# Kernel optimization log

Measured on AMD Instinct MI355X. Metric: run time of the kernel, lower is better.

The kernel has to match this reference:

```python
import jax, jax.numpy as jnp
import numpy as np

TEMP = 0.5  # init kwarg `tmp`
NUM_CLASSES = 100


def setup_inputs() -> dict:
    key = jax.random.key(0)
    k1, k2 = jax.random.split(key)
    embedding = jax.random.normal(k1, (8192, 256), dtype=jnp.float32)
    label = jax.random.randint(k2, (8192,), 0, NUM_CLASSES, dtype=jnp.int64)
    return {"embedding": embedding, "label": label}


def reference(embedding, label):
    # Row-normalize -> pairwise cosine similarity [N, N]
    normed = embedding / jnp.linalg.norm(embedding, axis=1, keepdims=True)
    sim = (normed @ normed.T) / TEMP  # already divided by temperature

    N = embedding.shape[0]
    eye = jnp.eye(N, dtype=bool)

    # Denominator: sum of exp(sim) over off-diagonal entries per row
    exp_sim = jnp.exp(sim)
    row_sum = jnp.sum(jnp.where(eye, 0.0, exp_sim), axis=1)  # [N]

    # log(exp(sim_ij) / row_sum_i) = sim_ij - log(row_sum_i)
    log_prob = sim - jnp.log(row_sum)[:, None]

    # Positive mask: same label, i != j
    pos_mask = (label[:, None] == label[None, :]) & ~eye
    n_i = jnp.sum(pos_mask, axis=1)  # positives per anchor

    inner = jnp.sum(jnp.where(pos_mask, log_prob, 0.0), axis=1)  # [N]
    per_anchor = jnp.where(n_i > 0, -inner / jnp.maximum(n_i, 1).astype(sim.dtype), 0.0)
    return jnp.sum(per_anchor)
```

## Files before the change

### kernel.cpp

```cpp
#include <hip/hip_runtime.h>
#include <hip/hip_bf16.h>
#include <stdint.h>

#define N    8192
#define D    256
#define NCLS 100

static constexpr float TEMP    = 0.5f;
static constexpr float SCALE_F = 1.69864360f;
static constexpr float LN2     = 0.69314718055994531f;

typedef float f32x4 __attribute__((ext_vector_type(4)));

__device__ __forceinline__ unsigned short f2bf(float f) {
  union { float f; unsigned int u; } x; x.f = f;
  unsigned int r = x.u + 0x7fffu + ((x.u >> 16) & 1u);
  return (unsigned short)(r >> 16);
}
__device__ __forceinline__ float bf2f(unsigned short b) {
  union { unsigned int u; float f; } x; x.u = ((unsigned int)b) << 16;
  return x.f;
}
__device__ __forceinline__ void gld16(const void* g, void* l) {
  __builtin_amdgcn_global_load_lds(
      (const __attribute__((address_space(1))) unsigned int*)g,
      (__attribute__((address_space(3))) unsigned int*)l, 16, 0, 0);
}


__global__ __launch_bounds__(256) void normalize_kernel(
    const float* __restrict__ emb, const long long* __restrict__ label,
    unsigned short* __restrict__ abf, unsigned char* __restrict__ a8,
    float* __restrict__ rowsum, int* __restrict__ cnt,
    int* __restrict__ list) {
  const int row  = blockIdx.x * 4 + (threadIdx.x >> 6);
  const int lane = threadIdx.x & 63;
  const float4 v = ((const float4*)(emb + (size_t)row * D))[lane];
  float ss = v.x * v.x + v.y * v.y + v.z * v.z + v.w * v.w;
#pragma unroll
  for (int off = 1; off < 64; off <<= 1) ss += __shfl_xor(ss, off);
  const float s = rsqrtf(ss) * SCALE_F;
  const float x = v.x * s, y = v.y * s, z = v.z * s, wv = v.w * s;

  ushort4 o;
  o.x = f2bf(x); o.y = f2bf(y); o.z = f2bf(z); o.w = f2bf(wv);
  ((ushort4*)(abf + (size_t)row * D))[lane] = o;

  int p = __builtin_amdgcn_cvt_pk_fp8_f32(x, y, 0, false);
  p = __builtin_amdgcn_cvt_pk_fp8_f32(z, wv, p, true);
  *(int*)(a8 + (size_t)(row >> 4) * 4096 + (lane >> 1) * 128 +
          (row & 15) * 8 + (lane & 1) * 4) = p;

  if (lane == 0) {
    rowsum[row] = 0.f;
    const int c = (int)label[row];
    const int slot = atomicAdd(cnt + c, 1);
    list[c * 256 + slot] = row;
  }
}

#define TM 128
#define TN 128
#define JT 4

__global__ __launch_bounds__(256, 3) void simexp_rowsum_kernel(
    const unsigned char* __restrict__ A, float* __restrict__ rowsum) {
  __shared__ __align__(16) unsigned char sa[TM * 256];
  const int tid  = threadIdx.x;
  const int w    = tid >> 6;
  const int lane = tid & 63;
  const int quad = lane >> 4;
  const int l15  = lane & 15;

  const int b = blockIdx.x;
  int x = (int)((-1.0f + sqrtf(1.0f + 2.0f * (float)b)) * 0.5f);
  while (2 * (x + 1) * (x + 1) + 2 * (x + 1) <= b) ++x;
  while (2 * x * x + 2 * x > b) --x;
  const int y = b - (2 * x * x + 2 * x);

  const int row0 = y * TM;
  const int jc0  = x * (TN * JT);
  const int sdiag = (y >= 4 * x) ? (y - 4 * x) : -1;
  const int jt0   = (sdiag >= 0) ? sdiag : 0;
  const int pr0 = row0 >> 4;
  const int pam = (w & 1) * 4;
  const int pbn = (w >> 1) * 4;
  const int wm  = (w & 1) * 64;
  const int jn0 = (w >> 1) * 64;

#pragma unroll
  for (int p = 0; p < 8; ++p) {
    const int seg = w * 8 + p;
    gld16(A + (size_t)(pr0 + (seg >> 2)) * 4096 + (seg & 3) * 1024 + lane * 16,
          sa + seg * 1024);
  }
  __syncthreads();

  float rowpart[4][4];
#pragma unroll
  for (int mt = 0; mt < 4; ++mt)
#pragma unroll
    for (int e = 0; e < 4; ++e) rowpart[mt][e] = 0.f;

  for (int jt = jt0; jt < JT; ++jt) {
    const unsigned char* Bp =
        A + (size_t)(((jc0 + jt * TN) >> 4) + pbn) * 4096;

    f32x4 acc[4][4];
#pragma unroll
    for (int mt = 0; mt < 4; ++mt)
#pragma unroll
      for (int nt = 0; nt < 4; ++nt) acc[mt][nt] = (f32x4){0.f, 0.f, 0.f, 0.f};

#pragma unroll
    for (int kq = 0; kq < 4; ++kq) {
#pragma unroll
      for (int kkl = 0; kkl < 2; ++kkl) {
        const int fo = (kkl * 4 + quad) * 128 + l15 * 8;
        long af[4], bf[4];
#pragma unroll
        for (int nt = 0; nt < 4; ++nt)
          bf[nt] = *(const long*)(Bp + nt * 4096 + kq * 1024 + fo);
#pragma unroll
        for (int mt = 0; mt < 4; ++mt)
          af[mt] = *(const long*)(sa + (pam + mt) * 4096 + kq * 1024 + fo);
#pragma unroll
        for (int mt = 0; mt < 4; ++mt)
#pragma unroll
          for (int nt = 0; nt < 4; ++nt)
            acc[mt][nt] = __builtin_amdgcn_mfma_f32_16x16x32_fp8_fp8(
                af[mt], bf[nt], acc[mt][nt], 0, 0, 0);
      }
    }

    const bool diag = (jt == sdiag);
    float colpart[4] = {0.f, 0.f, 0.f, 0.f};
#pragma unroll
    for (int mt = 0; mt < 4; ++mt)
#pragma unroll
      for (int nt = 0; nt < 4; ++nt)
#pragma unroll
        for (int e = 0; e < 4; ++e) {
          float v = __builtin_amdgcn_exp2f(acc[mt][nt][e]);
          if (diag) {
            const int iloc = wm + mt * 16 + quad * 4 + e;
            const int jloc = jn0 + nt * 16 + l15;
            v = (iloc < jloc) ? v : 0.f;
          }
          rowpart[mt][e] += v;
          colpart[nt] += v;
        }
#pragma unroll
    for (int nt = 0; nt < 4; ++nt) {
      float v = colpart[nt];
      v += __shfl_xor(v, 16);
      v += __shfl_xor(v, 32);
      if (quad == 0)
        atomicAdd(&rowsum[jc0 + jt * TN + jn0 + nt * 16 + l15], v);
    }
  }

#pragma unroll
  for (int mt = 0; mt < 4; ++mt)
#pragma unroll
    for (int e = 0; e < 4; ++e) {
      float v = rowpart[mt][e];
      v += __shfl_xor(v, 1);
      v += __shfl_xor(v, 2);
      v += __shfl_xor(v, 4);
      v += __shfl_xor(v, 8);
      if (l15 == 0)
        atomicAdd(&rowsum[row0 + wm + mt * 16 + quad * 4 + e], v);
    }
}

__global__ __launch_bounds__(256) void finalize_kernel(
    const unsigned short* __restrict__ abf, const float* __restrict__ rowsum,
    const long long* __restrict__ label, const int* __restrict__ cnt,
    const int* __restrict__ list, float* __restrict__ out) {
  __shared__ float red[4];
  __shared__ int rows_l[256];
  const int tid  = threadIdx.x;
  const int w    = tid >> 6;
  const int lane = tid & 63;

  if (blockIdx.x < NCLS) {
    const int c = blockIdx.x;
    const int m = cnt[c];
    if (m <= 1) return;
    if (tid < m) rows_l[tid] = list[c * 256 + tid];
    __syncthreads();
    float acc = 0.f;
    for (int s = 0; s < m; ++s)
      acc += bf2f(abf[(size_t)rows_l[s] * D + tid]);
    float v = acc * acc;
#pragma unroll
    for (int off = 1; off < 64; off <<= 1) v += __shfl_xor(v, off);
    if (lane == 0) red[w] = v;
    __syncthreads();
    if (tid == 0) {
      const float ssq = red[0] + red[1] + red[2] + red[3];
      const float term = (ssq * LN2 - 2.0f * (float)m) / (float)(m - 1);
      atomicAdd(out, -term);
    }
  } else {
    const int i = (blockIdx.x - NCLS) * 256 + tid;
    const int c = (int)label[i];
    float v = 0.f;
    if (cnt[c] > 1)
      v = __builtin_amdgcn_logf(rowsum[i]) * LN2;
#pragma unroll
    for (int off = 1; off < 64; off <<= 1) v += __shfl_xor(v, off);
    if (lane == 0) red[w] = v;
    __syncthreads();
    if (tid == 0)
      atomicAdd(out, red[0] + red[1] + red[2] + red[3]);
  }
}

extern "C" void kernel_launch(void* const* d_in, const int* in_sizes, int n_in,
                              void* d_out, int out_size, void* d_ws,
                              size_t ws_size, hipStream_t stream) {
  const float* emb = (const float*)d_in[0];
  const long long* label = (const long long*)d_in[1];
  float* out = (float*)d_out;

  char* ws = (char*)d_ws;
  unsigned short* abf = (unsigned short*)ws;
  unsigned char* a8 = (unsigned char*)(ws + (size_t)N * D * 2);
  float* rowsum = (float*)(ws + (size_t)N * D * 3);
  int* cnt = (int*)(rowsum + N);
  int* list = cnt + 128;

  hipMemsetAsync(cnt, 0, 128 * 4, stream);
  hipMemsetAsync(out, 0, sizeof(float), stream);

  normalize_kernel<<<N / 4, 256, 0, stream>>>(emb, label, abf, a8, rowsum,
                                              cnt, list);

  simexp_rowsum_kernel<<<544, 256, 0, stream>>>(a8, rowsum);

  finalize_kernel<<<NCLS + N / 256, 256, 0, stream>>>(abf, rowsum, label, cnt,
                                                      list, out);
}
```

Before: 129.9 us.

## Use one 128x128 triangle tile per block, dropping LDS staging

The similarity kernel now launches one block per 128x128 upper-triangular tile instead of blocks that each sweep four column tiles. The A operand is read directly from global memory rather than staged in LDS, and occupancy is raised to 4 blocks per CU. On diagonal tiles, the wave below the diagonal exits early and only the diagonal waves apply masking. This trades A-tile reuse across column tiles for more parallelism and less shared memory. The cost is more global/L2 traffic and more atomics on rowsum.

```diff
diff --git a/kernel.cpp b/kernel.cpp
--- a/kernel.cpp
+++ b/kernel.cpp
@@ -20,11 +20,6 @@
 __device__ __forceinline__ float bf2f(unsigned short b) {
   union { unsigned int u; float f; } x; x.u = ((unsigned int)b) << 16;
   return x.f;
-}
-__device__ __forceinline__ void gld16(const void* g, void* l) {
-  __builtin_amdgcn_global_load_lds(
-      (const __attribute__((address_space(1))) unsigned int*)g,
-      (__attribute__((address_space(3))) unsigned int*)l, 16, 0, 0);
 }
 
 
@@ -59,13 +54,8 @@
   }
 }
 
-#define TM 128
-#define TN 128
-#define JT 4
-
-__global__ __launch_bounds__(256, 3) void simexp_rowsum_kernel(
+__global__ __launch_bounds__(256, 4) void simexp_rowsum_kernel(
     const unsigned char* __restrict__ A, float* __restrict__ rowsum) {
-  __shared__ __align__(16) unsigned char sa[TM * 256];
   const int tid  = threadIdx.x;
   const int w    = tid >> 6;
   const int lane = tid & 63;
@@ -73,93 +63,79 @@
   const int l15  = lane & 15;
 
   const int b = blockIdx.x;
-  int x = (int)((-1.0f + sqrtf(1.0f + 2.0f * (float)b)) * 0.5f);
-  while (2 * (x + 1) * (x + 1) + 2 * (x + 1) <= b) ++x;
-  while (2 * x * x + 2 * x > b) --x;
-  const int y = b - (2 * x * x + 2 * x);
-
-  const int row0 = y * TM;
-  const int jc0  = x * (TN * JT);
-  const int sdiag = (y >= 4 * x) ? (y - 4 * x) : -1;
-  const int jt0   = (sdiag >= 0) ? sdiag : 0;
-  const int pr0 = row0 >> 4;
-  const int pam = (w & 1) * 4;
-  const int pbn = (w >> 1) * 4;
+  int x = (int)((-1.0f + sqrtf(1.0f + 8.0f * (float)b)) * 0.5f);
+  while ((x + 1) * (x + 2) / 2 <= b) ++x;
+  while (x * (x + 1) / 2 > b) --x;
+  const int y = b - x * (x + 1) / 2;
+
+  const int row0 = y << 7;
+  const int col0 = x << 7;
+  const bool diag = (x == y);
   const int wm  = (w & 1) * 64;
   const int jn0 = (w >> 1) * 64;
-
-#pragma unroll
-  for (int p = 0; p < 8; ++p) {
-    const int seg = w * 8 + p;
-    gld16(A + (size_t)(pr0 + (seg >> 2)) * 4096 + (seg & 3) * 1024 + lane * 16,
-          sa + seg * 1024);
-  }
-  __syncthreads();
+  if (diag && wm > jn0) return;
+  const bool needmask = diag && (wm == jn0);
+
+  const unsigned char* Ap = A + (size_t)((row0 >> 4) + (w & 1) * 4) * 4096;
+  const unsigned char* Bp = A + (size_t)((col0 >> 4) + (w >> 1) * 4) * 4096;
+
+  f32x4 acc[4][4];
+#pragma unroll
+  for (int mt = 0; mt < 4; ++mt)
+#pragma unroll
+    for (int nt = 0; nt < 4; ++nt) acc[mt][nt] = (f32x4){0.f, 0.f, 0.f, 0.f};
+
+#pragma unroll
+  for (int kq = 0; kq < 4; ++kq) {
+#pragma unroll
+    for (int kkl = 0; kkl < 2; ++kkl) {
+      const int fo = kq * 1024 + (kkl * 4 + quad) * 128 + l15 * 8;
+      long af[4], bf[4];
+#pragma unroll
+      for (int mt = 0; mt < 4; ++mt)
+        af[mt] = *(const long*)(Ap + mt * 4096 + fo);
+#pragma unroll
+      for (int nt = 0; nt < 4; ++nt)
+        bf[nt] = *(const long*)(Bp + nt * 4096 + fo);
+#pragma unroll
+      for (int mt = 0; mt < 4; ++mt)
+#pragma unroll
+        for (int nt = 0; nt < 4; ++nt)
+          acc[mt][nt] = __builtin_amdgcn_mfma_f32_16x16x32_fp8_fp8(
+              af[mt], bf[nt], acc[mt][nt], 0, 0, 0);
+    }
+  }
 
   float rowpart[4][4];
+  float colpart[4] = {0.f, 0.f, 0.f, 0.f};
 #pragma unroll
   for (int mt = 0; mt < 4; ++mt)
 #pragma unroll
     for (int e = 0; e < 4; ++e) rowpart[mt][e] = 0.f;
-
-  for (int jt = jt0; jt < JT; ++jt) {
-    const unsigned char* Bp =
-        A + (size_t)(((jc0 + jt * TN) >> 4) + pbn) * 4096;
-
-    f32x4 acc[4][4];
-#pragma unroll
-    for (int mt = 0; mt < 4; ++mt)
-#pragma unroll
-      for (int nt = 0; nt < 4; ++nt) acc[mt][nt] = (f32x4){0.f, 0.f, 0.f, 0.f};
-
-#pragma unroll
-    for (int kq = 0; kq < 4; ++kq) {
-#pragma unroll
-      for (int kkl = 0; kkl < 2; ++kkl) {
-        const int fo = (kkl * 4 + quad) * 128 + l15 * 8;
-        long af[4], bf[4];
-#pragma unroll
-        for (int nt = 0; nt < 4; ++nt)
-          bf[nt] = *(const long*)(Bp + nt * 4096 + kq * 1024 + fo);
-#pragma unroll
-        for (int mt = 0; mt < 4; ++mt)
-          af[mt] = *(const long*)(sa + (pam + mt) * 4096 + kq * 1024 + fo);
-#pragma unroll
-        for (int mt = 0; mt < 4; ++mt)
-#pragma unroll
-          for (int nt = 0; nt < 4; ++nt)
-            acc[mt][nt] = __builtin_amdgcn_mfma_f32_16x16x32_fp8_fp8(
-                af[mt], bf[nt], acc[mt][nt], 0, 0, 0);
+#pragma unroll
+  for (int mt = 0; mt < 4; ++mt)
+#pragma unroll
+    for (int nt = 0; nt < 4; ++nt)
+#pragma unroll
+      for (int e = 0; e < 4; ++e) {
+        float v = __builtin_amdgcn_exp2f(acc[mt][nt][e]);
+        if (needmask) {
+          const int iw = mt * 16 + quad * 4 + e;
+          const int jw = nt * 16 + l15;
+          v = (iw < jw) ? v : 0.f;
+        }
+        rowpart[mt][e] += v;
+        colpart[nt] += v;
       }
-    }
-
-    const bool diag = (jt == sdiag);
-    float colpart[4] = {0.f, 0.f, 0.f, 0.f};
-#pragma unroll
-    for (int mt = 0; mt < 4; ++mt)
-#pragma unroll
-      for (int nt = 0; nt < 4; ++nt)
-#pragma unroll
-        for (int e = 0; e < 4; ++e) {
-          float v = __builtin_amdgcn_exp2f(acc[mt][nt][e]);
-          if (diag) {
-            const int iloc = wm + mt * 16 + quad * 4 + e;
-            const int jloc = jn0 + nt * 16 + l15;
-            v = (iloc < jloc) ? v : 0.f;
-          }
-          rowpart[mt][e] += v;
-          colpart[nt] += v;
-        }
-#pragma unroll
-    for (int nt = 0; nt < 4; ++nt) {
-      float v = colpart[nt];
-      v += __shfl_xor(v, 16);
-      v += __shfl_xor(v, 32);
-      if (quad == 0)
-        atomicAdd(&rowsum[jc0 + jt * TN + jn0 + nt * 16 + l15], v);
-    }
-  }
-
+
+#pragma unroll
+  for (int nt = 0; nt < 4; ++nt) {
+    float v = colpart[nt];
+    v += __shfl_xor(v, 16);
+    v += __shfl_xor(v, 32);
+    if (quad == 0)
+      atomicAdd(&rowsum[col0 + jn0 + nt * 16 + l15], v);
+  }
 #pragma unroll
   for (int mt = 0; mt < 4; ++mt)
 #pragma unroll
@@ -238,7 +214,7 @@
   normalize_kernel<<<N / 4, 256, 0, stream>>>(emb, label, abf, a8, rowsum,
                                               cnt, list);
 
-  simexp_rowsum_kernel<<<544, 256, 0, stream>>>(a8, rowsum);
+  simexp_rowsum_kernel<<<2080, 256, 0, stream>>>(a8, rowsum);
 
   finalize_kernel<<<NCLS + N / 256, 256, 0, stream>>>(abf, rowsum, label, cnt,
                                                       list, out);
```

Measured after the change: 135.9 us. 1.05x slower.
